# Kernel tuning notes

Measured on AMD Instinct MI355X. Metric: run time of the kernel, lower is better.

## Reference

```python
import jax, jax.numpy as jnp
import numpy as np

B, D, C = 2048, 128, 100000
M, S, EPS = 0.3, 30.0, 0.1  # margin, scale, label smoothing


def setup_inputs() -> dict:
    key = jax.random.key(0)
    k1, k2, k3 = jax.random.split(key, 3)
    features = jax.random.normal(k1, (B, D), dtype=jnp.float32)
    labels = jax.random.randint(k2, (B,), 0, C, dtype=jnp.int64)
    weight = jax.random.normal(k3, (C, D), dtype=jnp.float32)  # nn.Linear weight (C, d)
    return {"features": features, "labels": labels, "weight": weight}


def reference(features, labels, weight):
    # L2-normalize features (rows) and classifier weight rows
    f = features / jnp.linalg.norm(features, axis=1, keepdims=True)
    w = weight / jnp.linalg.norm(weight, axis=1, keepdims=True)
    # cosine similarities, clamped to [-1, 1]
    cos = jnp.clip(jnp.einsum('bd,cd->bc', f, w), -1.0, 1.0)
    # subtract margin m at the label position for each sample (vectorized scatter)
    cos = cos.at[jnp.arange(B), labels].add(-M)
    logits = S * cos
    # label-smoothed cross entropy (mean reduction), matching torch semantics:
    # loss_i = (1-eps) * (-logp[i, y_i]) + eps * mean_c(-logp[i, c])
    logp = jax.nn.log_softmax(logits, axis=-1)
    nll = -jnp.take_along_axis(logp, labels[:, None], axis=1)[:, 0]
    smooth = -jnp.mean(logp, axis=-1)
    loss = jnp.mean((1.0 - EPS) * nll + EPS * smooth)
    return loss
```

## Files before the change

### kernel.cpp

```cpp
#include <hip/hip_runtime.h>
#include <stdint.h>
#include <math.h>

#define B_SZ   2048
#define D_SZ   128
#define C_SZ   100000
#define S_SC   30.0f
#define C2LOG  43.2808512f
#define M2LOG  12.9837726f
#define A_QS   173.1234048f
#define B_QS   256.0f
#define SCL_A  0x7D7D7D7Du
#define SCL_B  0x77777777u

#define BM     128
#define BN     64
#define NSUB   16
#define CPB    (BN*NSUB)
#define GRID_C ((C_SZ + CPB - 1)/CPB)
#define C_PAD  (GRID_C*CPB)
#define POST_SUB 3488.0f
#define NSLOT  (GRID_C*2)

typedef float f32x4 __attribute__((ext_vector_type(4)));
typedef int   i32x4 __attribute__((ext_vector_type(4)));
typedef int   i32x8 __attribute__((ext_vector_type(8)));
typedef unsigned char u8;

__device__ __forceinline__ void gload_lds16(const void* g, void* l) {
  __builtin_amdgcn_global_load_lds(
      (const __attribute__((address_space(1))) void*)g,
      (__attribute__((address_space(3))) void*)l, 16, 0, 0);
}

__global__ void rownorm_fp8_kernel(const float* __restrict__ in,
                                   u8* __restrict__ out, int rows,
                                   int valid_rows, float scale) {
  int row  = (blockIdx.x * blockDim.x + threadIdx.x) >> 6;
  int lane = threadIdx.x & 63;
  if (row >= rows) return;
  if (row >= valid_rows) {
    ((unsigned short*)(out + (size_t)row * D_SZ))[lane] = 0;
    return;
  }
  float2 v = ((const float2*)(in + (size_t)row * D_SZ))[lane];
  float ss = v.x * v.x + v.y * v.y;
  #pragma unroll
  for (int m = 1; m < 64; m <<= 1) ss += __shfl_xor(ss, m, 64);
  float rn = scale / sqrtf(ss);
  int pk = __builtin_amdgcn_cvt_pk_fp8_f32(v.x * rn, v.y * rn, 0, false);
  ((unsigned short*)(out + (size_t)row * D_SZ))[lane] = (unsigned short)(pk & 0xFFFF);
}

__global__ void labeldot_kernel(const float* __restrict__ f,
                                const int* __restrict__ labels,
                                const float* __restrict__ w,
                                float* __restrict__ cosy) {
  int row  = (blockIdx.x * blockDim.x + threadIdx.x) >> 6;
  int lane = threadIdx.x & 63;
  if (row >= B_SZ) return;
  int y = labels[row];
  float2 fv = ((const float2*)(f + (size_t)row * D_SZ))[lane];
  float2 wv = ((const float2*)(w + (size_t)y   * D_SZ))[lane];
  float d  = fv.x * wv.x + fv.y * wv.y;
  float ff = fv.x * fv.x + fv.y * fv.y;
  float ww = wv.x * wv.x + wv.y * wv.y;
  #pragma unroll
  for (int m = 1; m < 64; m <<= 1) {
    d  += __shfl_xor(d,  m, 64);
    ff += __shfl_xor(ff, m, 64);
    ww += __shfl_xor(ww, m, 64);
  }
  if (lane == 0) {
    float c = d / (sqrtf(ff) * sqrtf(ww));
    c = fminf(1.0f, fmaxf(-1.0f, c));
    cosy[row] = c;
  }
}

__global__ __launch_bounds__(256, 4) void gemm_partial_kernel(
    const u8* __restrict__ fn, const u8* __restrict__ wn,
    float* __restrict__ ps) {
  __shared__ __align__(16) u8 lds[2][BN * D_SZ];
  u8* flat = &lds[0][0];

  const int tid  = threadIdx.x;
  const int lane = tid & 63;
  const int wid  = tid >> 6;
  const int wr   = wid >> 1, wc = wid & 1;
  const int cb   = blockIdx.y;
  const int r0   = blockIdx.x * BM;
  const int hi   = lane >> 4;
  const int l15  = lane & 15;

  #pragma unroll
  for (int it = 0; it < 4; ++it) {
    int idx  = it * 256 + tid;
    int r    = idx >> 3;
    int s    = (idx & 7) ^ (r & 7);
    int wch  = it * 256 + (tid & ~63);
    gload_lds16(fn + (size_t)(r0 + r) * D_SZ + s * 16, flat + wch * 16);
  }
  asm volatile("s_waitcnt vmcnt(0)" ::: "memory");
  __builtin_amdgcn_s_barrier();

  i32x8 afrag[4];
  #pragma unroll
  for (int i = 0; i < 4; ++i) {
    int row = wr * 64 + i * 16 + l15;
    int s0  = (hi * 2)     ^ (row & 7);
    int s1  = (hi * 2 + 1) ^ (row & 7);
    i32x4 lo = *(const i32x4*)&flat[row * D_SZ + s0 * 16];
    i32x4 h4 = *(const i32x4*)&flat[row * D_SZ + s1 * 16];
    afrag[i] = __builtin_shufflevector(lo, h4, 0, 1, 2, 3, 4, 5, 6, 7);
  }
  asm volatile("s_waitcnt lgkmcnt(0)" ::: "memory");
  __builtin_amdgcn_s_barrier();

  const u8* bsrc[2];
  int wch[2];
  #pragma unroll
  for (int it = 0; it < 2; ++it) {
    int idx = it * 256 + tid;
    int cl  = idx >> 3;
    int s   = (idx & 7) ^ (cl & 7);
    bsrc[it] = wn + (size_t)(cb * CPB + cl) * D_SZ + s * 16;
    wch[it]  = it * 256 + (tid & ~63);
  }
  int boff[2][2];
  #pragma unroll
  for (int j = 0; j < 2; ++j) {
    int col = wc * 32 + j * 16 + l15;
    boff[j][0] = col * D_SZ + (((hi * 2)     ^ (col & 7)) * 16);
    boff[j][1] = col * D_SZ + (((hi * 2 + 1) ^ (col & 7)) * 16);
  }

  #pragma unroll
  for (int it = 0; it < 2; ++it)
    gload_lds16(bsrc[it], &lds[1][wch[it] * 16]);

  float sacc[4][4] = {};
  f32x4 acc1[4] = {};
  const f32x4 zero4 = {0.f, 0.f, 0.f, 0.f};

  #pragma unroll 1
  for (int sub = 0; sub < NSUB; ++sub) {
    asm volatile("s_waitcnt vmcnt(0)" ::: "memory");
    __builtin_amdgcn_s_barrier();

    if (sub < NSUB - 1) {
      u8* dst = &lds[sub & 1][0];
      #pragma unroll
      for (int it = 0; it < 2; ++it) {
        bsrc[it] += BN * D_SZ;
        gload_lds16(bsrc[it], dst + wch[it] * 16);
      }
    }

    const u8* bbuf = &lds[(sub + 1) & 1][0];

    i32x8 b0;
    {
      i32x4 lo = *(const i32x4*)&bbuf[boff[0][0]];
      i32x4 h4 = *(const i32x4*)&bbuf[boff[0][1]];
      b0 = __builtin_shufflevector(lo, h4, 0, 1, 2, 3, 4, 5, 6, 7);
    }
    f32x4 acc0[4];
    __builtin_amdgcn_s_setprio(1);
    #pragma unroll
    for (int i = 0; i < 4; ++i)
      acc0[i] = __builtin_amdgcn_mfma_scale_f32_16x16x128_f8f6f4(
          afrag[i], b0, zero4, 0, 0, 0, SCL_A, 0, SCL_B);
    __builtin_amdgcn_s_setprio(0);
    #pragma unroll
    for (int i = 0; i < 4; ++i) {
      f32x4 a4 = acc1[i];
      #pragma unroll
      for (int r = 0; r < 4; ++r)
        sacc[i][r] += __builtin_amdgcn_exp2f(a4[r]);
    }

    i32x8 b1;
    {
      i32x4 lo = *(const i32x4*)&bbuf[boff[1][0]];
      i32x4 h4 = *(const i32x4*)&bbuf[boff[1][1]];
      b1 = __builtin_shufflevector(lo, h4, 0, 1, 2, 3, 4, 5, 6, 7);
    }
    __builtin_amdgcn_s_setprio(1);
    #pragma unroll
    for (int i = 0; i < 4; ++i)
      acc1[i] = __builtin_amdgcn_mfma_scale_f32_16x16x128_f8f6f4(
          afrag[i], b1, zero4, 0, 0, 0, SCL_A, 0, SCL_B);
    __builtin_amdgcn_s_setprio(0);
    #pragma unroll
    for (int i = 0; i < 4; ++i) {
      f32x4 a4 = acc0[i];
      #pragma unroll
      for (int r = 0; r < 4; ++r)
        sacc[i][r] += __builtin_amdgcn_exp2f(a4[r]);
    }
  }

  #pragma unroll
  for (int i = 0; i < 4; ++i) {
    f32x4 a4 = acc1[i];
    #pragma unroll
    for (int r = 0; r < 4; ++r)
      sacc[i][r] += __builtin_amdgcn_exp2f(a4[r]);
  }

  #pragma unroll
  for (int i = 0; i < 4; ++i)
    #pragma unroll
    for (int r = 0; r < 4; ++r) {
      float s = sacc[i][r];
      #pragma unroll
      for (int m = 1; m < 16; m <<= 1) s += __shfl_xor(s, m, 64);
      if (l15 == 0) {
        int rowg = r0 + wr * 64 + i * 16 + hi * 4 + r;
        ps[(size_t)rowg * NSLOT + cb * 2 + wc] = s;
      }
    }
}

__global__ void merge_kernel(const float* __restrict__ ps,
                             const float* __restrict__ cosy,
                             float* __restrict__ losses) {
  int row  = (blockIdx.x * blockDim.x + threadIdx.x) >> 6;
  int lane = threadIdx.x & 63;
  if (row >= B_SZ) return;
  float s = 0.0f;
  for (int k = lane; k < NSLOT; k += 64) s += ps[(size_t)row * NSLOT + k];
  #pragma unroll
  for (int m = 1; m < 64; m <<= 1) s += __shfl_xor(s, m, 64);
  if (lane == 0) {
    float cy  = cosy[row];
    float zy2 = C2LOG * cy;
    s = s - POST_SUB - exp2f(zy2) + exp2f(zy2 - M2LOG);
    s = fmaxf(s, 1e-30f);
    float lse = logf(s);
    losses[row] = lse - 0.9f * (S_SC * cy - 9.0f);
  }
}

__global__ void final_kernel(const float* __restrict__ losses, float* __restrict__ out) {
  __shared__ float red[256];
  int tid = threadIdx.x;
  float s = 0.0f;
  for (int k = tid; k < B_SZ; k += 256) s += losses[k];
  red[tid] = s;
  __syncthreads();
  for (int off = 128; off > 0; off >>= 1) {
    if (tid < off) red[tid] += red[tid + off];
    __syncthreads();
  }
  if (tid == 0) out[0] = red[0] / (float)B_SZ;
}

extern "C" void kernel_launch(void* const* d_in, const int* in_sizes, int n_in,
                              void* d_out, int out_size, void* d_ws, size_t ws_size,
                              hipStream_t stream) {
  const float* feat   = (const float*)d_in[0];
  const int*   labels = (const int*)d_in[1];
  const float* weight = (const float*)d_in[2];
  float* out = (float*)d_out;

  char* ws = (char*)d_ws;
  size_t off = 0;
  u8* wn = (u8*)(ws + off);          off += (size_t)C_PAD * D_SZ;
  off = (off + 255) & ~(size_t)255;
  u8* fn = (u8*)(ws + off);          off += (size_t)B_SZ * D_SZ;
  off = (off + 255) & ~(size_t)255;
  float* cosy = (float*)(ws + off);  off += (size_t)B_SZ * 4;
  off = (off + 255) & ~(size_t)255;
  float* ps = (float*)(ws + off);    off += (size_t)B_SZ * NSLOT * 4;
  off = (off + 255) & ~(size_t)255;
  float* losses = (float*)(ws + off);

  rownorm_fp8_kernel<<<(C_PAD + 3) / 4, 256, 0, stream>>>(weight, wn, C_PAD, C_SZ, B_QS);
  rownorm_fp8_kernel<<<(B_SZ + 3) / 4, 256, 0, stream>>>(feat, fn, B_SZ, B_SZ, A_QS);
  labeldot_kernel<<<(B_SZ + 3) / 4, 256, 0, stream>>>(feat, labels, weight, cosy);

  dim3 grid(B_SZ / BM, GRID_C);
  gemm_partial_kernel<<<grid, 256, 0, stream>>>(fn, wn, ps);

  merge_kernel<<<(B_SZ + 3) / 4, 256, 0, stream>>>(ps, cosy, losses);
  final_kernel<<<1, 256, 0, stream>>>(losses, out);
}
```

Before: 66.58 us.

## Enlarge GEMM tile to 256x128 with 512 threads and fuse feature prep kernels

The fused GEMM+exp-sum kernel moves to 256-row by 128-column tiles with 8 waves per block and 8 sub-iterations. Each wave now processes four B fragments per sub-step, with ping-pong accumulators so the exp2 epilogue overlaps the MFMAs. This improves operand reuse and reduces the block count. Feature normalisation/FP8 packing is fused with the label-dot kernel, saving one launch and one read of the features. The trade-off is larger blocks and higher register and LDS pressure, with fewer column blocks available for load balance.

```diff
diff --git a/kernel.cpp b/kernel.cpp
--- a/kernel.cpp
+++ b/kernel.cpp
@@ -13,9 +13,9 @@
 #define SCL_A  0x7D7D7D7Du
 #define SCL_B  0x77777777u
 
-#define BM     128
-#define BN     64
-#define NSUB   16
+#define BM     256
+#define BN     128
+#define NSUB   8
 #define CPB    (BN*NSUB)
 #define GRID_C ((C_SZ + CPB - 1)/CPB)
 #define C_PAD  (GRID_C*CPB)
@@ -52,23 +52,28 @@
   ((unsigned short*)(out + (size_t)row * D_SZ))[lane] = (unsigned short)(pk & 0xFFFF);
 }
 
-__global__ void labeldot_kernel(const float* __restrict__ f,
-                                const int* __restrict__ labels,
-                                const float* __restrict__ w,
-                                float* __restrict__ cosy) {
+__global__ void prep_f_kernel(const float* __restrict__ f,
+                              const int* __restrict__ labels,
+                              const float* __restrict__ w,
+                              u8* __restrict__ fn, float* __restrict__ cosy) {
   int row  = (blockIdx.x * blockDim.x + threadIdx.x) >> 6;
   int lane = threadIdx.x & 63;
   if (row >= B_SZ) return;
+  float2 fv = ((const float2*)(f + (size_t)row * D_SZ))[lane];
+  float ff = fv.x * fv.x + fv.y * fv.y;
+  #pragma unroll
+  for (int m = 1; m < 64; m <<= 1) ff += __shfl_xor(ff, m, 64);
+  float rn = A_QS / sqrtf(ff);
+  int pk = __builtin_amdgcn_cvt_pk_fp8_f32(fv.x * rn, fv.y * rn, 0, false);
+  ((unsigned short*)(fn + (size_t)row * D_SZ))[lane] = (unsigned short)(pk & 0xFFFF);
+
   int y = labels[row];
-  float2 fv = ((const float2*)(f + (size_t)row * D_SZ))[lane];
-  float2 wv = ((const float2*)(w + (size_t)y   * D_SZ))[lane];
+  float2 wv = ((const float2*)(w + (size_t)y * D_SZ))[lane];
   float d  = fv.x * wv.x + fv.y * wv.y;
-  float ff = fv.x * fv.x + fv.y * fv.y;
   float ww = wv.x * wv.x + wv.y * wv.y;
   #pragma unroll
   for (int m = 1; m < 64; m <<= 1) {
     d  += __shfl_xor(d,  m, 64);
-    ff += __shfl_xor(ff, m, 64);
     ww += __shfl_xor(ww, m, 64);
   }
   if (lane == 0) {
@@ -78,7 +83,7 @@
   }
 }
 
-__global__ __launch_bounds__(256, 4) void gemm_partial_kernel(
+__global__ __launch_bounds__(512, 4) void gemm_partial_kernel(
     const u8* __restrict__ fn, const u8* __restrict__ wn,
     float* __restrict__ ps) {
   __shared__ __align__(16) u8 lds[2][BN * D_SZ];
@@ -95,10 +100,10 @@
 
   #pragma unroll
   for (int it = 0; it < 4; ++it) {
-    int idx  = it * 256 + tid;
+    int idx  = it * 512 + tid;
     int r    = idx >> 3;
     int s    = (idx & 7) ^ (r & 7);
-    int wch  = it * 256 + (tid & ~63);
+    int wch  = it * 512 + (tid & ~63);
     gload_lds16(fn + (size_t)(r0 + r) * D_SZ + s * 16, flat + wch * 16);
   }
   asm volatile("s_waitcnt vmcnt(0)" ::: "memory");
@@ -118,30 +123,53 @@
   __builtin_amdgcn_s_barrier();
 
   const u8* bsrc[2];
-  int wch[2];
+  int wch2[2];
   #pragma unroll
   for (int it = 0; it < 2; ++it) {
-    int idx = it * 256 + tid;
+    int idx = it * 512 + tid;
     int cl  = idx >> 3;
     int s   = (idx & 7) ^ (cl & 7);
     bsrc[it] = wn + (size_t)(cb * CPB + cl) * D_SZ + s * 16;
-    wch[it]  = it * 256 + (tid & ~63);
-  }
-  int boff[2][2];
-  #pragma unroll
-  for (int j = 0; j < 2; ++j) {
-    int col = wc * 32 + j * 16 + l15;
+    wch2[it] = it * 512 + (tid & ~63);
+  }
+  int boff[4][2];
+  #pragma unroll
+  for (int j = 0; j < 4; ++j) {
+    int col = wc * 64 + j * 16 + l15;
     boff[j][0] = col * D_SZ + (((hi * 2)     ^ (col & 7)) * 16);
     boff[j][1] = col * D_SZ + (((hi * 2 + 1) ^ (col & 7)) * 16);
   }
 
   #pragma unroll
   for (int it = 0; it < 2; ++it)
-    gload_lds16(bsrc[it], &lds[1][wch[it] * 16]);
+    gload_lds16(bsrc[it], &lds[1][wch2[it] * 16]);
 
   float sacc[4][4] = {};
-  f32x4 acc1[4] = {};
+  f32x4 accA[4];
+  f32x4 accB[4] = {};
   const f32x4 zero4 = {0.f, 0.f, 0.f, 0.f};
+
+#define LOADB(J, DEST)                                                        \
+  {                                                                           \
+    i32x4 lo = *(const i32x4*)&bbuf[boff[J][0]];                              \
+    i32x4 h4 = *(const i32x4*)&bbuf[boff[J][1]];                              \
+    DEST = __builtin_shufflevector(lo, h4, 0, 1, 2, 3, 4, 5, 6, 7);           \
+  }
+#define MFMA4(BF, ACC)                                                        \
+  __builtin_amdgcn_s_setprio(1);                                              \
+  _Pragma("unroll")                                                           \
+  for (int i = 0; i < 4; ++i)                                                 \
+    ACC[i] = __builtin_amdgcn_mfma_scale_f32_16x16x128_f8f6f4(                \
+        afrag[i], BF, zero4, 0, 0, 0, SCL_A, 0, SCL_B);                       \
+  __builtin_amdgcn_s_setprio(0);
+#define EPI(ACC)                                                              \
+  _Pragma("unroll")                                                           \
+  for (int i = 0; i < 4; ++i) {                                               \
+    f32x4 a4 = ACC[i];                                                        \
+    _Pragma("unroll")                                                         \
+    for (int r = 0; r < 4; ++r)                                               \
+      sacc[i][r] += __builtin_amdgcn_exp2f(a4[r]);                            \
+  }
 
   #pragma unroll 1
   for (int sub = 0; sub < NSUB; ++sub) {
@@ -153,61 +181,18 @@
       #pragma unroll
       for (int it = 0; it < 2; ++it) {
         bsrc[it] += BN * D_SZ;
-        gload_lds16(bsrc[it], dst + wch[it] * 16);
+        gload_lds16(bsrc[it], dst + wch2[it] * 16);
       }
     }
 
     const u8* bbuf = &lds[(sub + 1) & 1][0];
-
-    i32x8 b0;
-    {
-      i32x4 lo = *(const i32x4*)&bbuf[boff[0][0]];
-      i32x4 h4 = *(const i32x4*)&bbuf[boff[0][1]];
-      b0 = __builtin_shufflevector(lo, h4, 0, 1, 2, 3, 4, 5, 6, 7);
-    }
-    f32x4 acc0[4];
-    __builtin_amdgcn_s_setprio(1);
-    #pragma unroll
-    for (int i = 0; i < 4; ++i)
-      acc0[i] = __builtin_amdgcn_mfma_scale_f32_16x16x128_f8f6f4(
-          afrag[i], b0, zero4, 0, 0, 0, SCL_A, 0, SCL_B);
-    __builtin_amdgcn_s_setprio(0);
-    #pragma unroll
-    for (int i = 0; i < 4; ++i) {
-      f32x4 a4 = acc1[i];
-      #pragma unroll
-      for (int r = 0; r < 4; ++r)
-        sacc[i][r] += __builtin_amdgcn_exp2f(a4[r]);
-    }
-
-    i32x8 b1;
-    {
-      i32x4 lo = *(const i32x4*)&bbuf[boff[1][0]];
-      i32x4 h4 = *(const i32x4*)&bbuf[boff[1][1]];
-      b1 = __builtin_shufflevector(lo, h4, 0, 1, 2, 3, 4, 5, 6, 7);
-    }
-    __builtin_amdgcn_s_setprio(1);
-    #pragma unroll
-    for (int i = 0; i < 4; ++i)
-      acc1[i] = __builtin_amdgcn_mfma_scale_f32_16x16x128_f8f6f4(
-          afrag[i], b1, zero4, 0, 0, 0, SCL_A, 0, SCL_B);
-    __builtin_amdgcn_s_setprio(0);
-    #pragma unroll
-    for (int i = 0; i < 4; ++i) {
-      f32x4 a4 = acc0[i];
-      #pragma unroll
-      for (int r = 0; r < 4; ++r)
-        sacc[i][r] += __builtin_amdgcn_exp2f(a4[r]);
-    }
-  }
-
-  #pragma unroll
-  for (int i = 0; i < 4; ++i) {
-    f32x4 a4 = acc1[i];
-    #pragma unroll
-    for (int r = 0; r < 4; ++r)
-      sacc[i][r] += __builtin_amdgcn_exp2f(a4[r]);
-  }
+    i32x8 bf;
+    LOADB(0, bf); MFMA4(bf, accA); EPI(accB);
+    LOADB(1, bf); MFMA4(bf, accB); EPI(accA);
+    LOADB(2, bf); MFMA4(bf, accA); EPI(accB);
+    LOADB(3, bf); MFMA4(bf, accB); EPI(accA);
+  }
+  EPI(accB);
 
   #pragma unroll
   for (int i = 0; i < 4; ++i)
@@ -221,6 +206,9 @@
         ps[(size_t)rowg * NSLOT + cb * 2 + wc] = s;
       }
     }
+#undef LOADB
+#undef MFMA4
+#undef EPI
 }
 
 __global__ void merge_kernel(const float* __restrict__ ps,
@@ -278,11 +266,10 @@
   float* losses = (float*)(ws + off);
 
   rownorm_fp8_kernel<<<(C_PAD + 3) / 4, 256, 0, stream>>>(weight, wn, C_PAD, C_SZ, B_QS);
-  rownorm_fp8_kernel<<<(B_SZ + 3) / 4, 256, 0, stream>>>(feat, fn, B_SZ, B_SZ, A_QS);
-  labeldot_kernel<<<(B_SZ + 3) / 4, 256, 0, stream>>>(feat, labels, weight, cosy);
+  prep_f_kernel<<<(B_SZ + 3) / 4, 256, 0, stream>>>(feat, labels, weight, fn, cosy);
 
   dim3 grid(B_SZ / BM, GRID_C);
-  gemm_partial_kernel<<<grid, 256, 0, stream>>>(fn, wn, ps);
+  gemm_partial_kernel<<<grid, 512, 0, stream>>>(fn, wn, ps);
 
   merge_kernel<<<(B_SZ + 3) / 4, 256, 0, stream>>>(ps, cosy, losses);
   final_kernel<<<1, 256, 0, stream>>>(losses, out);
```

Result: slower. 169.9 us (+155.2%).

## Triple-buffer weight tiles in GEMM and fuse feature normalization with label dot

Applied to the files above, without the earlier changes.

The GEMM kernel moves from two to three LDS buffers for weight tiles and issues the first weight-tile loads alongside the feature-tile load. It waits with vmcnt(2) instead of draining all loads, so the load for the next-but-one tile stays in flight during compute. Separately, the feature fp8 normalization and the label cosine kernel are merged into one kernel, which removes one launch and one pass over the features. LDS use grows by 8KB per block, which may limit occupancy under the 4-blocks-per-SM launch bound.

```diff
diff --git a/kernel.cpp b/kernel.cpp
--- a/kernel.cpp
+++ b/kernel.cpp
@@ -52,23 +52,28 @@
   ((unsigned short*)(out + (size_t)row * D_SZ))[lane] = (unsigned short)(pk & 0xFFFF);
 }
 
-__global__ void labeldot_kernel(const float* __restrict__ f,
-                                const int* __restrict__ labels,
-                                const float* __restrict__ w,
-                                float* __restrict__ cosy) {
+__global__ void prep_f_kernel(const float* __restrict__ f,
+                              const int* __restrict__ labels,
+                              const float* __restrict__ w,
+                              u8* __restrict__ fn, float* __restrict__ cosy) {
   int row  = (blockIdx.x * blockDim.x + threadIdx.x) >> 6;
   int lane = threadIdx.x & 63;
   if (row >= B_SZ) return;
+  float2 fv = ((const float2*)(f + (size_t)row * D_SZ))[lane];
+  float ff = fv.x * fv.x + fv.y * fv.y;
+  #pragma unroll
+  for (int m = 1; m < 64; m <<= 1) ff += __shfl_xor(ff, m, 64);
+  float rn = A_QS / sqrtf(ff);
+  int pk = __builtin_amdgcn_cvt_pk_fp8_f32(fv.x * rn, fv.y * rn, 0, false);
+  ((unsigned short*)(fn + (size_t)row * D_SZ))[lane] = (unsigned short)(pk & 0xFFFF);
+
   int y = labels[row];
-  float2 fv = ((const float2*)(f + (size_t)row * D_SZ))[lane];
-  float2 wv = ((const float2*)(w + (size_t)y   * D_SZ))[lane];
+  float2 wv = ((const float2*)(w + (size_t)y * D_SZ))[lane];
   float d  = fv.x * wv.x + fv.y * wv.y;
-  float ff = fv.x * fv.x + fv.y * fv.y;
   float ww = wv.x * wv.x + wv.y * wv.y;
   #pragma unroll
   for (int m = 1; m < 64; m <<= 1) {
     d  += __shfl_xor(d,  m, 64);
-    ff += __shfl_xor(ff, m, 64);
     ww += __shfl_xor(ww, m, 64);
   }
   if (lane == 0) {
@@ -81,8 +86,7 @@
 __global__ __launch_bounds__(256, 4) void gemm_partial_kernel(
     const u8* __restrict__ fn, const u8* __restrict__ wn,
     float* __restrict__ ps) {
-  __shared__ __align__(16) u8 lds[2][BN * D_SZ];
-  u8* flat = &lds[0][0];
+  __shared__ __align__(16) u8 lds[3][BN * D_SZ];
 
   const int tid  = threadIdx.x;
   const int lane = tid & 63;
@@ -93,15 +97,31 @@
   const int hi   = lane >> 4;
   const int l15  = lane & 15;
 
+  const u8* bsrc[2];
+  int wch2[2];
+  #pragma unroll
+  for (int it = 0; it < 2; ++it) {
+    int idx = it * 256 + tid;
+    int cl  = idx >> 3;
+    int s   = (idx & 7) ^ (cl & 7);
+    bsrc[it] = wn + (size_t)(cb * CPB + cl) * D_SZ + s * 16;
+    wch2[it] = it * 256 + (tid & ~63);
+  }
+
+  u8* aflat = &lds[1][0];
   #pragma unroll
   for (int it = 0; it < 4; ++it) {
     int idx  = it * 256 + tid;
     int r    = idx >> 3;
     int s    = (idx & 7) ^ (r & 7);
     int wch  = it * 256 + (tid & ~63);
-    gload_lds16(fn + (size_t)(r0 + r) * D_SZ + s * 16, flat + wch * 16);
-  }
-  asm volatile("s_waitcnt vmcnt(0)" ::: "memory");
+    gload_lds16(fn + (size_t)(r0 + r) * D_SZ + s * 16, aflat + wch * 16);
+  }
+  #pragma unroll
+  for (int it = 0; it < 2; ++it)
+    gload_lds16(bsrc[it], &lds[0][wch2[it] * 16]);
+
+  asm volatile("s_waitcnt vmcnt(2)" ::: "memory");
   __builtin_amdgcn_s_barrier();
 
   i32x8 afrag[4];
@@ -110,23 +130,19 @@
     int row = wr * 64 + i * 16 + l15;
     int s0  = (hi * 2)     ^ (row & 7);
     int s1  = (hi * 2 + 1) ^ (row & 7);
-    i32x4 lo = *(const i32x4*)&flat[row * D_SZ + s0 * 16];
-    i32x4 h4 = *(const i32x4*)&flat[row * D_SZ + s1 * 16];
+    i32x4 lo = *(const i32x4*)&aflat[row * D_SZ + s0 * 16];
+    i32x4 h4 = *(const i32x4*)&aflat[row * D_SZ + s1 * 16];
     afrag[i] = __builtin_shufflevector(lo, h4, 0, 1, 2, 3, 4, 5, 6, 7);
   }
   asm volatile("s_waitcnt lgkmcnt(0)" ::: "memory");
   __builtin_amdgcn_s_barrier();
 
-  const u8* bsrc[2];
-  int wch[2];
   #pragma unroll
   for (int it = 0; it < 2; ++it) {
-    int idx = it * 256 + tid;
-    int cl  = idx >> 3;
-    int s   = (idx & 7) ^ (cl & 7);
-    bsrc[it] = wn + (size_t)(cb * CPB + cl) * D_SZ + s * 16;
-    wch[it]  = it * 256 + (tid & ~63);
-  }
+    bsrc[it] += BN * D_SZ;
+    gload_lds16(bsrc[it], &lds[1][wch2[it] * 16]);
+  }
+
   int boff[2][2];
   #pragma unroll
   for (int j = 0; j < 2; ++j) {
@@ -135,29 +151,30 @@
     boff[j][1] = col * D_SZ + (((hi * 2 + 1) ^ (col & 7)) * 16);
   }
 
-  #pragma unroll
-  for (int it = 0; it < 2; ++it)
-    gload_lds16(bsrc[it], &lds[1][wch[it] * 16]);
-
   float sacc[4][4] = {};
+  f32x4 acc0[4];
   f32x4 acc1[4] = {};
   const f32x4 zero4 = {0.f, 0.f, 0.f, 0.f};
 
   #pragma unroll 1
   for (int sub = 0; sub < NSUB; ++sub) {
-    asm volatile("s_waitcnt vmcnt(0)" ::: "memory");
+    if (sub < NSUB - 1) {
+      asm volatile("s_waitcnt vmcnt(2)" ::: "memory");
+    } else {
+      asm volatile("s_waitcnt vmcnt(0)" ::: "memory");
+    }
     __builtin_amdgcn_s_barrier();
 
-    if (sub < NSUB - 1) {
-      u8* dst = &lds[sub & 1][0];
+    if (sub < NSUB - 2) {
+      u8* dst = &lds[(sub + 2) % 3][0];
       #pragma unroll
       for (int it = 0; it < 2; ++it) {
         bsrc[it] += BN * D_SZ;
-        gload_lds16(bsrc[it], dst + wch[it] * 16);
+        gload_lds16(bsrc[it], dst + wch2[it] * 16);
       }
     }
 
-    const u8* bbuf = &lds[(sub + 1) & 1][0];
+    const u8* bbuf = &lds[sub % 3][0];
 
     i32x8 b0;
     {
@@ -165,7 +182,6 @@
       i32x4 h4 = *(const i32x4*)&bbuf[boff[0][1]];
       b0 = __builtin_shufflevector(lo, h4, 0, 1, 2, 3, 4, 5, 6, 7);
     }
-    f32x4 acc0[4];
     __builtin_amdgcn_s_setprio(1);
     #pragma unroll
     for (int i = 0; i < 4; ++i)
@@ -278,8 +294,7 @@
   float* losses = (float*)(ws + off);
 
   rownorm_fp8_kernel<<<(C_PAD + 3) / 4, 256, 0, stream>>>(weight, wn, C_PAD, C_SZ, B_QS);
-  rownorm_fp8_kernel<<<(B_SZ + 3) / 4, 256, 0, stream>>>(feat, fn, B_SZ, B_SZ, A_QS);
-  labeldot_kernel<<<(B_SZ + 3) / 4, 256, 0, stream>>>(feat, labels, weight, cosy);
+  prep_f_kernel<<<(B_SZ + 3) / 4, 256, 0, stream>>>(feat, labels, weight, fn, cosy);
 
   dim3 grid(B_SZ / BM, GRID_C);
   gemm_partial_kernel<<<grid, 256, 0, stream>>>(fn, wn, ps);
```

New measurement: 64.85 us. -2.6%, faster.
